# Kernel optimization log

Hardware: AMD Instinct MI355X
Metric: run time of the kernel (lower is better)

## Reference

```python
import jax, jax.numpy as jnp
import numpy as np

BATCH, NSTEPS, IN_F, OUT_F = 8192, 16, 256, 512


def setup_inputs() -> dict:
    key = jax.random.key(0)
    ks = jax.random.split(key, 20)
    r = jax.random.normal
    return {
        "x": r(ks[0], (BATCH, NSTEPS, IN_F), jnp.float32),
        "C": r(ks[1], (BATCH, OUT_F, 1), jnp.float32),
        "H": r(ks[2], (BATCH, OUT_F, 1), jnp.float32),
        "fg_w_c": r(ks[3], (OUT_F, 1), jnp.float32),
        "fg_w_h": r(ks[4], (OUT_F, OUT_F), jnp.float32),
        "fg_w_x": r(ks[5], (OUT_F, IN_F), jnp.float32),
        "fg_b": r(ks[6], (OUT_F, 1), jnp.float32),
        "ig_w_c": r(ks[7], (OUT_F, 1), jnp.float32),
        "ig_w_h": r(ks[8], (OUT_F, OUT_F), jnp.float32),
        "ig_w_x": r(ks[9], (OUT_F, IN_F), jnp.float32),
        "ig_b": r(ks[10], (OUT_F, 1), jnp.float32),
        "in_w_h": r(ks[11], (OUT_F, OUT_F), jnp.float32),
        "in_w_x": r(ks[12], (OUT_F, IN_F), jnp.float32),
        "in_b": r(ks[13], (OUT_F, 1), jnp.float32),
        "og_w_cn": r(ks[14], (OUT_F, 1), jnp.float32),
        "og_w_h": r(ks[15], (OUT_F, OUT_F), jnp.float32),
        "og_w_x": r(ks[16], (OUT_F, IN_F), jnp.float32),
        "og_b": r(ks[17], (OUT_F, 1), jnp.float32),
        "n": 3,
    }


def reference(x, C, H,
              fg_w_c, fg_w_h, fg_w_x, fg_b,
              ig_w_c, ig_w_h, ig_w_x, ig_b,
              in_w_h, in_w_x, in_b,
              og_w_cn, og_w_h, og_w_x, og_b,
              n):
    # x: [B, T, IN] -> current step [B, IN, 1]
    x_cur = x[:, n, :, None]
    # peephole LSTM gates; matmul broadcasts [O,O] @ [B,O,1] -> [B,O,1]
    fg = jax.nn.sigmoid(fg_w_c * C + jnp.matmul(fg_w_h, H) + jnp.matmul(fg_w_x, x_cur) + fg_b)
    ig = jax.nn.sigmoid(ig_w_c * C + jnp.matmul(ig_w_h, H) + jnp.matmul(ig_w_x, x_cur) + ig_b)
    inn = jnp.tanh(jnp.matmul(in_w_h, H) + jnp.matmul(in_w_x, x_cur) + in_b)
    cm = fg * C + ig * inn
    og = jax.nn.sigmoid(og_w_cn * cm + jnp.matmul(og_w_h, H) + jnp.matmul(og_w_x, x_cur) + og_b)
    h = og * jnp.tanh(cm)
    return (cm, h)
```

## Files before the change

### kernel.cpp

```cpp
#include <hip/hip_runtime.h>


typedef _Float16 half8 __attribute__((ext_vector_type(8)));
typedef _Float16 half4v __attribute__((ext_vector_type(4)));
typedef float floatx4 __attribute__((ext_vector_type(4)));

#define BATCH 8192
#define NSTEPS 16
#define IN_F 256
#define OUT_F 512
#define KDIM 768
#define NDIM 2048
#define HSIZE ((size_t)BATCH * OUT_F)

#define BM 128
#define BN 128
#define BK 64

__device__ __forceinline__ void async_copy16(const void* gptr, void* lptr) {
  __builtin_amdgcn_global_load_lds(
      (const __attribute__((address_space(1))) unsigned int*)gptr,
      (__attribute__((address_space(3))) unsigned int*)lptr,
      16, 0, 0);
}

__device__ __forceinline__ float sigmoidf_(float x) {
  return 1.0f / (1.0f + __expf(-x));
}

__device__ __forceinline__ float tanhf_(float x) {
  x = fminf(fmaxf(x, -20.0f), 20.0f);
  float e = __expf(2.0f * x);
  return (e - 1.0f) / (e + 1.0f);
}

__global__ void pack_AW(const float* __restrict__ H, const float* __restrict__ x,
                        const int* __restrict__ nptr,
                        const float* __restrict__ fg_w_h, const float* __restrict__ fg_w_x,
                        const float* __restrict__ ig_w_h, const float* __restrict__ ig_w_x,
                        const float* __restrict__ in_w_h, const float* __restrict__ in_w_x,
                        const float* __restrict__ og_w_h, const float* __restrict__ og_w_x,
                        _Float16* __restrict__ A, _Float16* __restrict__ W) {
  const int blk = blockIdx.x;
  const int k = threadIdx.x * 4;
  const float* src;
  _Float16* dst;
  if (blk < BATCH) {
    const int b = blk;
    if (k < OUT_F) {
      src = H + (size_t)b * OUT_F + k;
    } else {
      const int n = *nptr;
      src = x + ((size_t)b * NSTEPS + n) * IN_F + (k - OUT_F);
    }
    dst = A + (size_t)b * KDIM + k;
  } else {
    const int row = blk - BATCH;
    const int g  = (row >> 4) & 3;
    const int jj = ((row >> 6) << 4) | (row & 15);
    if (k < OUT_F) {
      const float* wh = (g == 0) ? fg_w_h : (g == 1) ? ig_w_h : (g == 2) ? in_w_h : og_w_h;
      src = wh + (size_t)jj * OUT_F + k;
    } else {
      const float* wx = (g == 0) ? fg_w_x : (g == 1) ? ig_w_x : (g == 2) ? in_w_x : og_w_x;
      src = wx + (size_t)jj * IN_F + (k - OUT_F);
    }
    dst = W + (size_t)row * KDIM + k;
  }
  float4 v = *(const float4*)src;
  half4v h = {(_Float16)v.x, (_Float16)v.y, (_Float16)v.z, (_Float16)v.w};
  *(half4v*)dst = h;
}

__global__ __launch_bounds__(256, 4) void gemm_lstm(
    const _Float16* __restrict__ A, const _Float16* __restrict__ W,
    const float* __restrict__ C,
    const float* __restrict__ fg_w_c, const float* __restrict__ fg_b,
    const float* __restrict__ ig_w_c, const float* __restrict__ ig_b,
    const float* __restrict__ in_b,
    const float* __restrict__ og_w_cn, const float* __restrict__ og_b,
    float* __restrict__ out) {
  __shared__ __align__(16) char smem[32768];
  _Float16* As = (_Float16*)smem;
  _Float16* Bs = (_Float16*)(smem + 16384);
  float* cmS = (float*)smem;
  float* hS  = (float*)(smem + 16384);

  const int tid = threadIdx.x;
  const int lane = tid & 63;
  const int wave = tid >> 6;
  const int quad = lane >> 4;
  const int l16 = lane & 15;
  const int m0 = blockIdx.y * BM;
  const int n0 = blockIdx.x * BN;
  const int mw = (wave >> 1) * 64;
  const int nw = (wave & 1) * 64;

  const int jj = (((n0 + nw) >> 6) << 4) | l16;
  const float fwc = fg_w_c[jj], fb = fg_b[jj];
  const float iwc = ig_w_c[jj], ib = ig_b[jj];
  const float nb  = in_b[jj];
  const float owc = og_w_cn[jj], ob = og_b[jj];

  floatx4 acc[4][4] = {};

  for (int kt = 0; kt < KDIM; kt += BK) {
    __syncthreads();
#pragma unroll
    for (int r = 0; r < 4; ++r) {
      const int g = r * 256 + tid;
      const int row = g >> 3;
      const int cl = g & 7;
      const int cg = cl ^ (row & 7);
      async_copy16(A + (size_t)(m0 + row) * KDIM + kt + cg * 8,
                   As + g * 8);
      async_copy16(W + (size_t)(n0 + row) * KDIM + kt + cg * 8,
                   Bs + g * 8);
    }
    __syncthreads();

#pragma unroll
    for (int ks = 0; ks < 2; ++ks) {
      half8 af[4], bf[4];
#pragma unroll
      for (int i = 0; i < 4; ++i) {
        const int row = mw + i * 16 + l16;
        const int chunk = ks * 4 + quad;
        const int gran = row * 8 + (chunk ^ (row & 7));
        af[i] = *(const half8*)(As + gran * 8);
      }
#pragma unroll
      for (int j = 0; j < 4; ++j) {
        const int row = nw + j * 16 + l16;
        const int chunk = ks * 4 + quad;
        const int gran = row * 8 + (chunk ^ (row & 7));
        bf[j] = *(const half8*)(Bs + gran * 8);
      }
#pragma unroll
      for (int i = 0; i < 4; ++i)
#pragma unroll
        for (int j = 0; j < 4; ++j)
          acc[i][j] = __builtin_amdgcn_mfma_f32_16x16x32_f16(af[i], bf[j], acc[i][j], 0, 0, 0);
    }
  }

  float cv[16];
#pragma unroll
  for (int i = 0; i < 4; ++i) {
    const int rbase = m0 + mw + i * 16 + quad * 4;
#pragma unroll
    for (int r = 0; r < 4; ++r)
      cv[i * 4 + r] = C[(size_t)(rbase + r) * OUT_F + jj];
  }
  float inn[16];
#pragma unroll
  for (int i = 0; i < 4; ++i)
#pragma unroll
    for (int r = 0; r < 4; ++r)
      inn[i * 4 + r] = tanhf_(acc[i][2][r] + nb);

  __syncthreads();

  const int jjloc = (nw >> 6) * 16 + l16;
#pragma unroll
  for (int i = 0; i < 4; ++i) {
    const int rloc0 = mw + i * 16 + quad * 4;
#pragma unroll
    for (int r = 0; r < 4; ++r) {
      const float c = cv[i * 4 + r];
      const float fg  = sigmoidf_(fwc * c + acc[i][0][r] + fb);
      const float ig  = sigmoidf_(iwc * c + acc[i][1][r] + ib);
      const float cm  = fg * c + ig * inn[i * 4 + r];
      const float og  = sigmoidf_(owc * cm + acc[i][3][r] + ob);
      cmS[(rloc0 + r) * 32 + jjloc] = cm;
      hS [(rloc0 + r) * 32 + jjloc] = og * tanhf_(cm);
    }
  }
  __syncthreads();

  const int bx32 = blockIdx.x * 32;
#pragma unroll
  for (int q = 0; q < 4; ++q) {
    const int idx = q * 256 + tid;
    const int row = idx >> 3;
    const int c4 = idx & 7;
    const size_t gbase = (size_t)(m0 + row) * OUT_F + bx32 + c4 * 4;
    *(float4*)(out + gbase) = *(const float4*)(cmS + row * 32 + c4 * 4);
    *(float4*)(out + HSIZE + gbase) = *(const float4*)(hS + row * 32 + c4 * 4);
  }
}

extern "C" void kernel_launch(void* const* d_in, const int* in_sizes, int n_in,
                              void* d_out, int out_size, void* d_ws, size_t ws_size,
                              hipStream_t stream) {
  const float* x       = (const float*)d_in[0];
  const float* C       = (const float*)d_in[1];
  const float* H       = (const float*)d_in[2];
  const float* fg_w_c  = (const float*)d_in[3];
  const float* fg_w_h  = (const float*)d_in[4];
  const float* fg_w_x  = (const float*)d_in[5];
  const float* fg_b    = (const float*)d_in[6];
  const float* ig_w_c  = (const float*)d_in[7];
  const float* ig_w_h  = (const float*)d_in[8];
  const float* ig_w_x  = (const float*)d_in[9];
  const float* ig_b    = (const float*)d_in[10];
  const float* in_w_h  = (const float*)d_in[11];
  const float* in_w_x  = (const float*)d_in[12];
  const float* in_b    = (const float*)d_in[13];
  const float* og_w_cn = (const float*)d_in[14];
  const float* og_w_h  = (const float*)d_in[15];
  const float* og_w_x  = (const float*)d_in[16];
  const float* og_b    = (const float*)d_in[17];
  const int*   nptr    = (const int*)d_in[18];

  char* ws = (char*)d_ws;
  _Float16* Apk = (_Float16*)ws;
  _Float16* Wpk = (_Float16*)(ws + 12582912);
  (void)ws_size; (void)in_sizes; (void)n_in; (void)out_size;

  pack_AW<<<BATCH + NDIM, 192, 0, stream>>>(H, x, nptr,
                                            fg_w_h, fg_w_x, ig_w_h, ig_w_x,
                                            in_w_h, in_w_x, og_w_h, og_w_x,
                                            Apk, Wpk);
  dim3 grid(NDIM / BN, BATCH / BM);
  gemm_lstm<<<grid, 256, 0, stream>>>(Apk, Wpk, C,
                                      fg_w_c, fg_b, ig_w_c, ig_b, in_b,
                                      og_w_cn, og_b, (float*)d_out);
}
```

Measured before the change: 256.1 us.

## Enlarge GEMM tiles to 256x256, double-buffer LDS, batch pack rows per block

The fused LSTM GEMM moves from 128x128 tiles with 256 threads to 256x256 tiles with 512 threads. Each wave now holds a 128x64 accumulator, which raises reuse per loaded fragment. LDS grows to 128KB so the next K tile can be loaded asynchronously while the current one is computed, leaving one barrier per iteration. The pack kernel now handles 8 rows per block to cut block count, but the larger tiles give only 256 GEMM blocks and use more registers and LDS, which may hurt occupancy.

```diff
diff --git a/kernel.cpp b/kernel.cpp
--- a/kernel.cpp
+++ b/kernel.cpp
@@ -13,9 +13,10 @@
 #define NDIM 2048
 #define HSIZE ((size_t)BATCH * OUT_F)
 
-#define BM 128
-#define BN 128
+#define BM 256
+#define BN 256
 #define BK 64
+#define NKT (KDIM / BK)
 
 __device__ __forceinline__ void async_copy16(const void* gptr, void* lptr) {
   __builtin_amdgcn_global_load_lds(
@@ -34,6 +35,7 @@
   return (e - 1.0f) / (e + 1.0f);
 }
 
+#define PACK_ROWS 8
 __global__ void pack_AW(const float* __restrict__ H, const float* __restrict__ x,
                         const int* __restrict__ nptr,
                         const float* __restrict__ fg_w_h, const float* __restrict__ fg_w_x,
@@ -41,38 +43,42 @@
                         const float* __restrict__ in_w_h, const float* __restrict__ in_w_x,
                         const float* __restrict__ og_w_h, const float* __restrict__ og_w_x,
                         _Float16* __restrict__ A, _Float16* __restrict__ W) {
-  const int blk = blockIdx.x;
   const int k = threadIdx.x * 4;
-  const float* src;
-  _Float16* dst;
-  if (blk < BATCH) {
-    const int b = blk;
-    if (k < OUT_F) {
-      src = H + (size_t)b * OUT_F + k;
+  const int n = *nptr;
+  const int row0 = blockIdx.x * PACK_ROWS;
+#pragma unroll
+  for (int rr = 0; rr < PACK_ROWS; ++rr) {
+    const int blk = row0 + rr;
+    const float* src;
+    _Float16* dst;
+    if (blk < BATCH) {
+      const int b = blk;
+      if (k < OUT_F) {
+        src = H + (size_t)b * OUT_F + k;
+      } else {
+        src = x + ((size_t)b * NSTEPS + n) * IN_F + (k - OUT_F);
+      }
+      dst = A + (size_t)b * KDIM + k;
     } else {
-      const int n = *nptr;
-      src = x + ((size_t)b * NSTEPS + n) * IN_F + (k - OUT_F);
-    }
-    dst = A + (size_t)b * KDIM + k;
-  } else {
-    const int row = blk - BATCH;
-    const int g  = (row >> 4) & 3;
-    const int jj = ((row >> 6) << 4) | (row & 15);
-    if (k < OUT_F) {
-      const float* wh = (g == 0) ? fg_w_h : (g == 1) ? ig_w_h : (g == 2) ? in_w_h : og_w_h;
-      src = wh + (size_t)jj * OUT_F + k;
-    } else {
-      const float* wx = (g == 0) ? fg_w_x : (g == 1) ? ig_w_x : (g == 2) ? in_w_x : og_w_x;
-      src = wx + (size_t)jj * IN_F + (k - OUT_F);
-    }
-    dst = W + (size_t)row * KDIM + k;
-  }
-  float4 v = *(const float4*)src;
-  half4v h = {(_Float16)v.x, (_Float16)v.y, (_Float16)v.z, (_Float16)v.w};
-  *(half4v*)dst = h;
-}
-
-__global__ __launch_bounds__(256, 4) void gemm_lstm(
+      const int row = blk - BATCH;
+      const int g  = (row >> 4) & 3;
+      const int jj = ((row >> 6) << 4) | (row & 15);
+      if (k < OUT_F) {
+        const float* wh = (g == 0) ? fg_w_h : (g == 1) ? ig_w_h : (g == 2) ? in_w_h : og_w_h;
+        src = wh + (size_t)jj * OUT_F + k;
+      } else {
+        const float* wx = (g == 0) ? fg_w_x : (g == 1) ? ig_w_x : (g == 2) ? in_w_x : og_w_x;
+        src = wx + (size_t)jj * IN_F + (k - OUT_F);
+      }
+      dst = W + (size_t)row * KDIM + k;
+    }
+    float4 v = *(const float4*)src;
+    half4v h = {(_Float16)v.x, (_Float16)v.y, (_Float16)v.z, (_Float16)v.w};
+    *(half4v*)dst = h;
+  }
+}
+
+__global__ __launch_bounds__(512, 2) void gemm_lstm(
     const _Float16* __restrict__ A, const _Float16* __restrict__ W,
     const float* __restrict__ C,
     const float* __restrict__ fg_w_c, const float* __restrict__ fg_b,
@@ -80,113 +86,110 @@
     const float* __restrict__ in_b,
     const float* __restrict__ og_w_cn, const float* __restrict__ og_b,
     float* __restrict__ out) {
-  __shared__ __align__(16) char smem[32768];
-  _Float16* As = (_Float16*)smem;
-  _Float16* Bs = (_Float16*)(smem + 16384);
-  float* cmS = (float*)smem;
-  float* hS  = (float*)(smem + 16384);
+  __shared__ __align__(16) char smem[131072];
 
   const int tid = threadIdx.x;
   const int lane = tid & 63;
   const int wave = tid >> 6;
   const int quad = lane >> 4;
   const int l16 = lane & 15;
+  const int wm = wave >> 2;
+  const int wn = wave & 3;
   const int m0 = blockIdx.y * BM;
   const int n0 = blockIdx.x * BN;
-  const int mw = (wave >> 1) * 64;
-  const int nw = (wave & 1) * 64;
-
-  const int jj = (((n0 + nw) >> 6) << 4) | l16;
+
+  const int jj = (((n0 + wn * 64) >> 6) << 4) | l16;
   const float fwc = fg_w_c[jj], fb = fg_b[jj];
   const float iwc = ig_w_c[jj], ib = ig_b[jj];
   const float nb  = in_b[jj];
   const float owc = og_w_cn[jj], ob = og_b[jj];
 
-  floatx4 acc[4][4] = {};
-
-  for (int kt = 0; kt < KDIM; kt += BK) {
-    __syncthreads();
+  floatx4 acc[8][4] = {};
+
+  auto stage = [&](int p, int kt) {
+    _Float16* As = (_Float16*)(smem + p * 65536);
+    _Float16* Bs = (_Float16*)(smem + p * 65536 + 32768);
 #pragma unroll
     for (int r = 0; r < 4; ++r) {
-      const int g = r * 256 + tid;
+      const int g = r * 512 + tid;
       const int row = g >> 3;
       const int cl = g & 7;
       const int cg = cl ^ (row & 7);
-      async_copy16(A + (size_t)(m0 + row) * KDIM + kt + cg * 8,
-                   As + g * 8);
-      async_copy16(W + (size_t)(n0 + row) * KDIM + kt + cg * 8,
-                   Bs + g * 8);
-    }
-    __syncthreads();
-
+      async_copy16(A + (size_t)(m0 + row) * KDIM + kt + cg * 8, As + g * 8);
+      async_copy16(W + (size_t)(n0 + row) * KDIM + kt + cg * 8, Bs + g * 8);
+    }
+  };
+
+  stage(0, 0);
+  __syncthreads();
+
+  int cur = 0;
+  for (int t = 0; t < NKT; ++t) {
+    if (t + 1 < NKT) stage(cur ^ 1, (t + 1) * BK);
+    const _Float16* As = (const _Float16*)(smem + cur * 65536);
+    const _Float16* Bs = (const _Float16*)(smem + cur * 65536 + 32768);
 #pragma unroll
     for (int ks = 0; ks < 2; ++ks) {
-      half8 af[4], bf[4];
-#pragma unroll
-      for (int i = 0; i < 4; ++i) {
-        const int row = mw + i * 16 + l16;
+      half8 af[8], bf[4];
+#pragma unroll
+      for (int j = 0; j < 4; ++j) {
+        const int row = wn * 64 + j * 16 + l16;
+        const int chunk = ks * 4 + quad;
+        const int gran = row * 8 + (chunk ^ (row & 7));
+        bf[j] = *(const half8*)(Bs + gran * 8);
+      }
+#pragma unroll
+      for (int i = 0; i < 8; ++i) {
+        const int row = wm * 128 + i * 16 + l16;
         const int chunk = ks * 4 + quad;
         const int gran = row * 8 + (chunk ^ (row & 7));
         af[i] = *(const half8*)(As + gran * 8);
       }
 #pragma unroll
-      for (int j = 0; j < 4; ++j) {
-        const int row = nw + j * 16 + l16;
-        const int chunk = ks * 4 + quad;
-        const int gran = row * 8 + (chunk ^ (row & 7));
-        bf[j] = *(const half8*)(Bs + gran * 8);
-      }
-#pragma unroll
-      for (int i = 0; i < 4; ++i)
+      for (int i = 0; i < 8; ++i)
 #pragma unroll
         for (int j = 0; j < 4; ++j)
           acc[i][j] = __builtin_amdgcn_mfma_f32_16x16x32_f16(af[i], bf[j], acc[i][j], 0, 0, 0);
     }
-  }
-
-  float cv[16];
-#pragma unroll
-  for (int i = 0; i < 4; ++i) {
-    const int rbase = m0 + mw + i * 16 + quad * 4;
+    __syncthreads();
+    cur ^= 1;
+  }
+
+  float* cmS = (float*)smem;
+  float* hS  = (float*)(smem + 65536);
+
+  const int jjloc = wn * 16 + l16;
+#pragma unroll
+  for (int i = 0; i < 8; ++i) {
+    const int rbase = m0 + wm * 128 + i * 16 + quad * 4;
+    float cv[4];
 #pragma unroll
     for (int r = 0; r < 4; ++r)
-      cv[i * 4 + r] = C[(size_t)(rbase + r) * OUT_F + jj];
-  }
-  float inn[16];
-#pragma unroll
-  for (int i = 0; i < 4; ++i)
-#pragma unroll
-    for (int r = 0; r < 4; ++r)
-      inn[i * 4 + r] = tanhf_(acc[i][2][r] + nb);
-
-  __syncthreads();
-
-  const int jjloc = (nw >> 6) * 16 + l16;
-#pragma unroll
-  for (int i = 0; i < 4; ++i) {
-    const int rloc0 = mw + i * 16 + quad * 4;
+      cv[r] = C[(size_t)(rbase + r) * OUT_F + jj];
 #pragma unroll
     for (int r = 0; r < 4; ++r) {
-      const float c = cv[i * 4 + r];
+      const float c = cv[r];
+      const float inn = tanhf_(acc[i][2][r] + nb);
       const float fg  = sigmoidf_(fwc * c + acc[i][0][r] + fb);
       const float ig  = sigmoidf_(iwc * c + acc[i][1][r] + ib);
-      const float cm  = fg * c + ig * inn[i * 4 + r];
+      const float cm  = fg * c + ig * inn;
       const float og  = sigmoidf_(owc * cm + acc[i][3][r] + ob);
-      cmS[(rloc0 + r) * 32 + jjloc] = cm;
-      hS [(rloc0 + r) * 32 + jjloc] = og * tanhf_(cm);
+      const int rloc = wm * 128 + i * 16 + quad * 4 + r;
+      cmS[rloc * 64 + jjloc] = cm;
+      hS [rloc * 64 + jjloc] = og * tanhf_(cm);
     }
   }
   __syncthreads();
 
-  const int bx32 = blockIdx.x * 32;
-#pragma unroll
-  for (int q = 0; q < 4; ++q) {
-    const int idx = q * 256 + tid;
-    const int row = idx >> 3;
-    const int c4 = idx & 7;
-    const size_t gbase = (size_t)(m0 + row) * OUT_F + bx32 + c4 * 4;
-    *(float4*)(out + gbase) = *(const float4*)(cmS + row * 32 + c4 * 4);
-    *(float4*)(out + HSIZE + gbase) = *(const float4*)(hS + row * 32 + c4 * 4);
+  const int ub = blockIdx.x * 64;
+#pragma unroll
+  for (int q = 0; q < 8; ++q) {
+    const int idx = q * 512 + tid;
+    const int row = idx >> 4;
+    const int c4 = idx & 15;
+    const size_t gbase = (size_t)(m0 + row) * OUT_F + ub + c4 * 4;
+    *(float4*)(out + gbase) = *(const float4*)(cmS + row * 64 + c4 * 4);
+    *(float4*)(out + HSIZE + gbase) = *(const float4*)(hS + row * 64 + c4 * 4);
   }
 }
 
@@ -218,12 +221,13 @@
   _Float16* Wpk = (_Float16*)(ws + 12582912);
   (void)ws_size; (void)in_sizes; (void)n_in; (void)out_size;
 
-  pack_AW<<<BATCH + NDIM, 192, 0, stream>>>(H, x, nptr,
-                                            fg_w_h, fg_w_x, ig_w_h, ig_w_x,
-                                            in_w_h, in_w_x, og_w_h, og_w_x,
-                                            Apk, Wpk);
+  pack_AW<<<(BATCH + NDIM) / PACK_ROWS, 192, 0, stream>>>(
+      H, x, nptr,
+      fg_w_h, fg_w_x, ig_w_h, ig_w_x,
+      in_w_h, in_w_x, og_w_h, og_w_x,
+      Apk, Wpk);
   dim3 grid(NDIM / BN, BATCH / BM);
-  gemm_lstm<<<grid, 256, 0, stream>>>(Apk, Wpk, C,
+  gemm_lstm<<<grid, 512, 0, stream>>>(Apk, Wpk, C,
                                       fg_w_c, fg_b, ig_w_c, ig_b, in_b,
                                       og_w_cn, og_b, (float*)d_out);
 }
```

After: 258.9 us. About the same (+1.1%).
